# Performance work log

Hardware: AMD Instinct MI355X
Metric: run time of the kernel (lower is better)

The kernel has to match this reference:

```python
import jax, jax.numpy as jnp
import numpy as np

N_NODES = 50000
N_EDGES = 800000
D_IN = 128
D_H = 128
D_OUT = 1
N_GRAPHS = 64
BN_EPS = 1e-5


def _lin(key, i, o):
    return jax.random.normal(key, (i, o), jnp.float32) / np.float32(np.sqrt(i))


def setup_inputs() -> dict:
    key = jax.random.key(0)
    ks = jax.random.split(key, 40)
    inp = {}
    inp["x"] = jax.random.normal(ks[0], (N_NODES, D_IN), jnp.float32)
    inp["edge_index"] = jax.random.randint(ks[1], (2, N_EDGES), 0, N_NODES)
    inp["batch"] = jnp.sort(jax.random.randint(ks[2], (N_NODES,), 0, N_GRAPHS))
    dims = [D_IN, D_H, D_H]
    ki = 3
    for l in range(3):
        inp[f"l{l}_W1"] = _lin(ks[ki], dims[l], D_H); ki += 1
        inp[f"l{l}_b1"] = jnp.zeros((D_H,), jnp.float32)
        inp[f"l{l}_W2"] = _lin(ks[ki], D_H, D_H); ki += 1
        inp[f"l{l}_b2"] = jnp.zeros((D_H,), jnp.float32)
        inp[f"l{l}_g"] = jnp.ones((D_H,), jnp.float32)
        inp[f"l{l}_beta"] = jnp.zeros((D_H,), jnp.float32)
    inp["p_W1"] = _lin(ks[ki], D_H * 3, D_H); ki += 1
    inp["p_b1"] = jnp.zeros((D_H,), jnp.float32)
    inp["p_g"] = jnp.ones((D_H,), jnp.float32)
    inp["p_beta"] = jnp.zeros((D_H,), jnp.float32)
    inp["p_W2"] = _lin(ks[ki], D_H, D_OUT); ki += 1
    inp["p_b2"] = jnp.zeros((D_OUT,), jnp.float32)
    return inp


def _bn(h, g, b):
    # training-mode BatchNorm1d: biased batch statistics over dim 0
    m = h.mean(0)
    v = h.var(0)
    return (h - m) * (g / jnp.sqrt(v + BN_EPS)) + b


def _gin_conv(x, src, dst, W1, b1, W2, b2):
    # scatter-add neighbor aggregation: messages x[src] summed into dst
    agg = jax.ops.segment_sum(x[src], dst, num_segments=N_NODES)
    h = x + agg  # eps = 0 (GINConv default)
    h = jax.nn.relu(h @ W1 + b1)
    return h @ W2 + b2


def reference(x, edge_index, batch,
              l0_W1, l0_b1, l0_W2, l0_b2, l0_g, l0_beta,
              l1_W1, l1_b1, l1_W2, l1_b2, l1_g, l1_beta,
              l2_W1, l2_b1, l2_W2, l2_b2, l2_g, l2_beta,
              p_W1, p_b1, p_g, p_beta, p_W2, p_b2):
    src, dst = edge_index[0], edge_index[1]
    layers = [
        (l0_W1, l0_b1, l0_W2, l0_b2, l0_g, l0_beta),
        (l1_W1, l1_b1, l1_W2, l1_b2, l1_g, l1_beta),
        (l2_W1, l2_b1, l2_W2, l2_b2, l2_g, l2_beta),
    ]
    h = x
    h_list = []
    for (W1, b1, W2, b2, g, beta) in layers:
        h = _gin_conv(h, src, dst, W1, b1, W2, b2)
        h = jax.nn.relu(_bn(h, g, beta))
        # dropout: identity in eval mode
        h_list.append(h)
    # global mean pool per layer, then concat
    cnt = jax.ops.segment_sum(jnp.ones((N_NODES,), jnp.float32), batch,
                              num_segments=N_GRAPHS)
    cnt = jnp.maximum(cnt, 1.0)[:, None]
    pooled = [jax.ops.segment_sum(hh, batch, num_segments=N_GRAPHS) / cnt
              for hh in h_list]
    z = jnp.concatenate(pooled, axis=1)  # [G, 3*D_H]
    # prediction MLP: fc1 -> relu -> bn -> fc2 (dropout identity)
    z = jax.nn.relu(z @ p_W1 + p_b1)
    z = _bn(z, p_g, p_beta)
    return z @ p_W2 + p_b2  # [G, D_OUT]
```

## Files before the change

kernel.cpp:

```cpp
#include <hip/hip_runtime.h>

#define NN 50000
#define NE 800000
#define D  128
#define NG 64
#define BN_EPS 1e-5f
#define SCAN_B 196

typedef __attribute__((ext_vector_type(8))) short short8;
typedef __attribute__((ext_vector_type(4))) float f32x4;

static __device__ inline unsigned short f2bf_rn(float f) {
  unsigned u = __float_as_uint(f);
  unsigned r = (u + 0x7FFF + ((u >> 16) & 1)) >> 16;
  return (unsigned short)r;
}
static __device__ inline float bf2f(unsigned short h) {
  return __uint_as_float((unsigned)h << 16);
}

__global__ void k_hist(const int* __restrict__ dst, int* __restrict__ counts) {
  int e = blockIdx.x * blockDim.x + threadIdx.x;
  if (e < NE) atomicAdd(&counts[dst[e]], 1);
}

__global__ void k_scan1(const int* __restrict__ counts, int* __restrict__ bsum) {
  const int t = threadIdx.x;
  const int i = blockIdx.x * 256 + t;
  int v = (i < NN) ? counts[i] : 0;
  #pragma unroll
  for (int d = 32; d >= 1; d >>= 1) v += __shfl_xor(v, d, 64);
  __shared__ int ws[4];
  if ((t & 63) == 0) ws[t >> 6] = v;
  __syncthreads();
  if (t == 0) bsum[blockIdx.x] = ws[0] + ws[1] + ws[2] + ws[3];
}

__global__ void k_scan2(const int* __restrict__ bsum, int* __restrict__ boff,
                        int* __restrict__ offs) {
  const int t = threadIdx.x, lane = t & 63, w = t >> 6;
  int v = (t < SCAN_B) ? bsum[t] : 0;
  int s = v;
  #pragma unroll
  for (int d = 1; d < 64; d <<= 1) { int u = __shfl_up(s, d, 64); if (lane >= d) s += u; }
  __shared__ int ws[4];
  if (lane == 63) ws[w] = s;
  __syncthreads();
  int add = 0;
  for (int k = 0; k < w; ++k) add += ws[k];
  if (t < SCAN_B) boff[t] = add + s - v;
  if (t == SCAN_B - 1) offs[NN] = add + s;
}

__global__ void k_scan3(const int* __restrict__ counts, const int* __restrict__ boff,
                        int* __restrict__ offs) {
  const int t = threadIdx.x, lane = t & 63, w = t >> 6;
  const int i = blockIdx.x * 256 + t;
  int v = (i < NN) ? counts[i] : 0;
  int s = v;
  #pragma unroll
  for (int d = 1; d < 64; d <<= 1) { int u = __shfl_up(s, d, 64); if (lane >= d) s += u; }
  __shared__ int ws[4];
  if (lane == 63) ws[w] = s;
  __syncthreads();
  int add = 0;
  for (int k = 0; k < w; ++k) add += ws[k];
  if (i < NN) offs[i] = boff[blockIdx.x] + add + s - v;
}

__global__ void k_scatter(const int* __restrict__ src, const int* __restrict__ dst,
                          const int* __restrict__ offs, int* __restrict__ cursor,
                          int* __restrict__ esrc) {
  int e = blockIdx.x * blockDim.x + threadIdx.x;
  if (e < NE) {
    int d = dst[e];
    int p = offs[d] + atomicAdd(&cursor[d], 1);
    esrc[p] = src[e];
  }
}

__global__ void k_gbounds(const int* __restrict__ batch, int* __restrict__ gstart) {
  const int g = threadIdx.x;
  if (g > NG) return;
  int lo = 0, hi = NN;
  while (lo < hi) { int mid = (lo + hi) >> 1; if (batch[mid] < g) lo = mid + 1; else hi = mid; }
  gstart[g] = lo;
}

__global__ __launch_bounds__(256) void k_cvt(const float* __restrict__ X,
                                             unsigned long long* __restrict__ Xb) {
  const int n4 = NN * D / 4;
  for (int i = blockIdx.x * blockDim.x + threadIdx.x; i < n4; i += gridDim.x * blockDim.x) {
    float4 v = ((const float4*)X)[i];
    unsigned long long p = (unsigned long long)f2bf_rn(v.x) |
                           ((unsigned long long)f2bf_rn(v.y) << 16) |
                           ((unsigned long long)f2bf_rn(v.z) << 32) |
                           ((unsigned long long)f2bf_rn(v.w) << 48);
    Xb[i] = p;
  }
}

struct WPtrs { const float* w[6]; };
__global__ void k_prep6(WPtrs ws, short* __restrict__ wb) {
  const int widx = blockIdx.y;
  const float* __restrict__ W = ws.w[widx];
  short* __restrict__ Wh = wb + (size_t)(widx * 2) * 16384;
  short* __restrict__ Wl = Wh + 16384;
  const int idx = blockIdx.x * 256 + threadIdx.x;
  const int k = idx >> 7, c = idx & 127;
  const float v = W[idx];
  const unsigned short h = f2bf_rn(v);
  const unsigned short lo = f2bf_rn(v - bf2f(h));
  const int o = ((k >> 5) * 128 + c) * 32 + (k & 31);
  Wh[o] = (short)h;
  Wl[o] = (short)lo;
}

template<bool BN>
__global__ __launch_bounds__(256) void k_aggregate(const unsigned* __restrict__ Hb,
                                                   const int* __restrict__ offs,
                                                   const int* __restrict__ esrc,
                                                   const float* __restrict__ scale,
                                                   const float* __restrict__ shift,
                                                   unsigned* __restrict__ AGGh,
                                                   unsigned* __restrict__ AGGl) {
  const int node = blockIdx.x * 4 + (threadIdx.x >> 6);
  const int lane = threadIdx.x & 63;
  float2 sc = make_float2(1.f, 1.f), sh = make_float2(0.f, 0.f);
  if (BN) { sc = ((const float2*)scale)[lane]; sh = ((const float2*)shift)[lane]; }

  auto rd = [&](int r) -> float2 {
    const unsigned u = Hb[r * 64 + lane];
    float2 v = make_float2(bf2f((unsigned short)u), bf2f((unsigned short)(u >> 16)));
    if (BN) {
      v.x = fmaxf(fmaf(v.x, sc.x, sh.x), 0.f);
      v.y = fmaxf(fmaf(v.y, sc.y, sh.y), 0.f);
    }
    return v;
  };

  float2 acc = rd(node);
  const int b = offs[node], e = offs[node + 1];
  int i = b;
  for (; i + 4 <= e; i += 4) {
    const int s0 = esrc[i], s1 = esrc[i + 1], s2 = esrc[i + 2], s3 = esrc[i + 3];
    const float2 v0 = rd(s0), v1 = rd(s1), v2 = rd(s2), v3 = rd(s3);
    acc.x += (v0.x + v1.x) + (v2.x + v3.x);
    acc.y += (v0.y + v1.y) + (v2.y + v3.y);
  }
  for (; i < e; ++i) {
    const float2 v = rd(esrc[i]);
    acc.x += v.x; acc.y += v.y;
  }
  const unsigned short hx = f2bf_rn(acc.x), hy = f2bf_rn(acc.y);
  AGGh[node * 64 + lane] = (unsigned)hx | ((unsigned)hy << 16);
  const unsigned short lx = f2bf_rn(acc.x - bf2f(hx)), ly = f2bf_rn(acc.y - bf2f(hy));
  AGGl[node * 64 + lane] = (unsigned)lx | ((unsigned)ly << 16);
}

__global__ __launch_bounds__(256, 3) void k_mlp(const short* __restrict__ AGGh,
                                                const short* __restrict__ AGGl,
                                                const short* __restrict__ W1h, const short* __restrict__ W1l,
                                                const short* __restrict__ W2h, const short* __restrict__ W2l,
                                                const float* __restrict__ b1, const float* __restrict__ b2,
                                                short* __restrict__ Hb,
                                                float* __restrict__ sums, float* __restrict__ sumsq) {
  __shared__ __align__(16) short sC1h[64 * 136];
  __shared__ __align__(16) short sC1l[64 * 136];

  const int t = threadIdx.x;
  const int l = t & 63, w = t >> 6;
  const int lr = l & 15, fq = l >> 4;
  const int lk = fq * 8;
  const int row0 = blockIdx.x * 64;
  const int arow = row0 + w * 16 + lr;
  const bool rowok = arow < NN;

  f32x4 acc[8];
  #pragma unroll
  for (int ct = 0; ct < 8; ++ct) acc[ct] = (f32x4)(0.f);
  #pragma unroll 1
  for (int kc = 0; kc < 4; ++kc) {
    short8 ah = (short8)(0), al = (short8)(0);
    if (rowok) {
      ah = *(const short8*)(AGGh + (size_t)arow * D + kc * 32 + lk);
      al = *(const short8*)(AGGl + (size_t)arow * D + kc * 32 + lk);
    }
    short8 bh[8], bl[8];
    #pragma unroll
    for (int ct = 0; ct < 8; ++ct) {
      bh[ct] = *(const short8*)(W1h + (kc * 128 + ct * 16 + lr) * 32 + lk);
      bl[ct] = *(const short8*)(W1l + (kc * 128 + ct * 16 + lr) * 32 + lk);
    }
    #pragma unroll
    for (int ct = 0; ct < 8; ++ct) {
      acc[ct] = __builtin_amdgcn_mfma_f32_16x16x32_bf16(ah, bh[ct], acc[ct], 0, 0, 0);
      acc[ct] = __builtin_amdgcn_mfma_f32_16x16x32_bf16(al, bh[ct], acc[ct], 0, 0, 0);
      acc[ct] = __builtin_amdgcn_mfma_f32_16x16x32_bf16(ah, bl[ct], acc[ct], 0, 0, 0);
    }
  }

  #pragma unroll
  for (int ct = 0; ct < 8; ++ct) {
    const float bb = b1[ct * 16 + lr];
    #pragma unroll
    for (int j = 0; j < 4; ++j) {
      const int r = w * 16 + fq * 4 + j;
      const float v = fmaxf(acc[ct][j] + bb, 0.f);
      const unsigned short h = f2bf_rn(v);
      sC1h[r * 136 + ct * 16 + lr] = (short)h;
      sC1l[r * 136 + ct * 16 + lr] = (short)f2bf_rn(v - bf2f(h));
    }
  }
  __syncthreads();

  f32x4 acc2[8];
  #pragma unroll
  for (int ct = 0; ct < 8; ++ct) acc2[ct] = (f32x4)(0.f);
  #pragma unroll 1
  for (int kc = 0; kc < 4; ++kc) {
    const short8 ah = *(const short8*)(sC1h + (w * 16 + lr) * 136 + kc * 32 + lk);
    const short8 al = *(const short8*)(sC1l + (w * 16 + lr) * 136 + kc * 32 + lk);
    short8 bh[8], bl[8];
    #pragma unroll
    for (int ct = 0; ct < 8; ++ct) {
      bh[ct] = *(const short8*)(W2h + (kc * 128 + ct * 16 + lr) * 32 + lk);
      bl[ct] = *(const short8*)(W2l + (kc * 128 + ct * 16 + lr) * 32 + lk);
    }
    #pragma unroll
    for (int ct = 0; ct < 8; ++ct) {
      acc2[ct] = __builtin_amdgcn_mfma_f32_16x16x32_bf16(ah, bh[ct], acc2[ct], 0, 0, 0);
      acc2[ct] = __builtin_amdgcn_mfma_f32_16x16x32_bf16(al, bh[ct], acc2[ct], 0, 0, 0);
      acc2[ct] = __builtin_amdgcn_mfma_f32_16x16x32_bf16(ah, bl[ct], acc2[ct], 0, 0, 0);
    }
  }

  float ps[8], pq[8];
  #pragma unroll
  for (int ct = 0; ct < 8; ++ct) { ps[ct] = 0.f; pq[ct] = 0.f; }
  #pragma unroll
  for (int ct = 0; ct < 8; ++ct) {
    const float bb = b2[ct * 16 + lr];
    #pragma unroll
    for (int j = 0; j < 4; ++j) {
      const int gr = row0 + w * 16 + fq * 4 + j;
      if (gr < NN) {
        const float v = acc2[ct][j] + bb;
        Hb[(size_t)gr * D + ct * 16 + lr] = (short)f2bf_rn(v);
        ps[ct] += v; pq[ct] += v * v;
      }
    }
  }
  __syncthreads();
  float* red  = (float*)sC1h;
  float* redq = (float*)sC1l;
  const int grp = w * 4 + fq;
  #pragma unroll
  for (int ct = 0; ct < 8; ++ct) {
    red [grp * 128 + ct * 16 + lr] = ps[ct];
    redq[grp * 128 + ct * 16 + lr] = pq[ct];
  }
  __syncthreads();
  if (t < 128) {
    float s = 0.f, q = 0.f;
    #pragma unroll
    for (int g2 = 0; g2 < 16; ++g2) { s += red[g2 * 128 + t]; q += redq[g2 * 128 + t]; }
    atomicAdd(&sums[t], s);
    atomicAdd(&sumsq[t], q);
  }
}

__global__ void k_stats(const float* __restrict__ sums, const float* __restrict__ sumsq,
                        const float* __restrict__ g, const float* __restrict__ beta,
                        float* __restrict__ scale, float* __restrict__ shift) {
  const int c = threadIdx.x;
  const float m   = sums[c] / (float)NN;
  const float var = sumsq[c] / (float)NN - m * m;
  const float sc  = g[c] / sqrtf(var + BN_EPS);
  scale[c] = sc;
  shift[c] = beta[c] - m * sc;
}

__global__ __launch_bounds__(256) void k_pool(const unsigned short* __restrict__ Hb,
                                              const float* __restrict__ scale,
                                              const float* __restrict__ shift,
                                              const int* __restrict__ gstart,
                                              float* __restrict__ pooled, int lofs) {
  const int g = blockIdx.y;
  const int s = gstart[g], e = gstart[g + 1];
  const int t = threadIdx.x, c = t & 127, half = t >> 7;
  const float sc = scale[c], sh = shift[c];
  const int len = e - s;
  const int nchunk = (int)gridDim.x;
  const int per = (len + nchunk - 1) / nchunk;
  const int r0 = s + (int)blockIdx.x * per;
  const int r1 = min(e, r0 + per);
  float sum = 0.f;
  for (int r = r0 + half; r < r1; r += 2)
    sum += fmaxf(fmaf(bf2f(Hb[r * D + c]), sc, sh), 0.f);
  __shared__ float red[256];
  red[t] = sum;
  __syncthreads();
  if (t < 128) atomicAdd(&pooled[g * 384 + lofs + c], red[t] + red[t + 128]);
}

__global__ __launch_bounds__(128) void k_fc1(const float* __restrict__ pooled,
                                             const int* __restrict__ gstart,
                                             const float* __restrict__ W1,
                                             const float* __restrict__ b1,
                                             float* __restrict__ z1) {
  const int g = blockIdx.x, j = threadIdx.x;
  __shared__ float p[384];
  const float cnt = (float)(gstart[g + 1] - gstart[g]);
  const float inv = 1.f / fmaxf(cnt, 1.f);
  for (int k = j; k < 384; k += 128) p[k] = pooled[g * 384 + k] * inv;
  __syncthreads();
  float acc = b1[j];
  #pragma unroll 8
  for (int k = 0; k < 384; ++k) acc = fmaf(p[k], W1[k * 128 + j], acc);
  z1[g * 128 + j] = fmaxf(acc, 0.f);
}

__global__ __launch_bounds__(128) void k_head(const float* __restrict__ z1,
                                              const float* __restrict__ g,
                                              const float* __restrict__ beta,
                                              const float* __restrict__ W2,
                                              const float* __restrict__ b2,
                                              float* __restrict__ out) {
  __shared__ float z2[NG][129];
  __shared__ float w2s[128];
  const int j = threadIdx.x;
  w2s[j] = W2[j];
  float vals[NG];
  float s = 0.f, q = 0.f;
  for (int gg = 0; gg < NG; ++gg) {
    float v = z1[gg * 128 + j];
    vals[gg] = v; s += v; q += v * v;
  }
  const float m   = s / (float)NG;
  const float var = q / (float)NG - m * m;
  const float sc  = g[j] / sqrtf(var + BN_EPS);
  const float sh  = beta[j] - m * sc;
  for (int gg = 0; gg < NG; ++gg) z2[gg][j] = vals[gg] * sc + sh;
  __syncthreads();
  if (j < NG) {
    float acc = b2[0];
    #pragma unroll 8
    for (int k = 0; k < 128; ++k) acc += z2[j][k] * w2s[k];
    out[j] = acc;
  }
}

extern "C" void kernel_launch(void* const* d_in, const int* in_sizes, int n_in,
                              void* d_out, int out_size, void* d_ws, size_t ws_size,
                              hipStream_t stream) {
  const float* x     = (const float*)d_in[0];
  const int*   e_src = (const int*)d_in[1];
  const int*   e_dst = e_src + NE;
  const int*   batch = (const int*)d_in[2];
  const float *lW1[3], *lb1[3], *lW2[3], *lb2[3], *lg[3], *lbeta[3];
  for (int l = 0; l < 3; ++l) {
    lW1[l]   = (const float*)d_in[3 + 6 * l + 0];
    lb1[l]   = (const float*)d_in[3 + 6 * l + 1];
    lW2[l]   = (const float*)d_in[3 + 6 * l + 2];
    lb2[l]   = (const float*)d_in[3 + 6 * l + 3];
    lg[l]    = (const float*)d_in[3 + 6 * l + 4];
    lbeta[l] = (const float*)d_in[3 + 6 * l + 5];
  }
  const float* pW1   = (const float*)d_in[21];
  const float* pb1   = (const float*)d_in[22];
  const float* pg    = (const float*)d_in[23];
  const float* pbeta = (const float*)d_in[24];
  const float* pW2   = (const float*)d_in[25];
  const float* pb2   = (const float*)d_in[26];
  float* out = (float*)d_out;

  char* w = (char*)d_ws;
  auto alloc = [&](size_t bytes) { char* p = w; w += (bytes + 255) & ~(size_t)255; return p; };
  short* AGGh   = (short*)alloc((size_t)NN * D * 2);
  short* AGGl   = (short*)alloc((size_t)NN * D * 2);
  short* Hb0    = (short*)alloc((size_t)NN * D * 2);
  short* Hb1    = (short*)alloc((size_t)NN * D * 2);
  short* xb     = Hb1;
  int*   counts = (int*)alloc((size_t)NN * 4);
  int*   cursor = (int*)alloc((size_t)NN * 4);
  int*   offs   = (int*)alloc((size_t)(NN + 1) * 4);
  int*   esrc   = (int*)alloc((size_t)NE * 4);
  int*   bsum   = (int*)alloc((size_t)SCAN_B * 4);
  int*   boff   = (int*)alloc((size_t)SCAN_B * 4);
  int*   gstart = (int*)alloc((size_t)(NG + 1) * 4);
  float* stats  = (float*)alloc((size_t)4 * 128 * 4);
  float* sums = stats, *sumsq = stats + 128, *scale = stats + 256, *shift = stats + 384;
  float* pooled = (float*)alloc((size_t)NG * 384 * 4);
  float* z1     = (float*)alloc((size_t)NG * 128 * 4);
  short* wb     = (short*)alloc((size_t)12 * 32768);

  hipMemsetAsync(counts, 0, (size_t)NN * 4, stream);
  hipMemsetAsync(cursor, 0, (size_t)NN * 4, stream);
  hipMemsetAsync(pooled, 0, (size_t)NG * 384 * 4, stream);

  k_hist   <<<(NE + 255) / 256, 256, 0, stream>>>(e_dst, counts);
  k_scan1  <<<SCAN_B, 256, 0, stream>>>(counts, bsum);
  k_scan2  <<<1, 256, 0, stream>>>(bsum, boff, offs);
  k_scan3  <<<SCAN_B, 256, 0, stream>>>(counts, boff, offs);
  k_scatter<<<(NE + 255) / 256, 256, 0, stream>>>(e_src, e_dst, offs, cursor, esrc);
  k_gbounds<<<1, 128, 0, stream>>>(batch, gstart);
  k_cvt    <<<1024, 256, 0, stream>>>(x, (unsigned long long*)xb);

  WPtrs ws;
  ws.w[0] = lW1[0]; ws.w[1] = lW2[0];
  ws.w[2] = lW1[1]; ws.w[3] = lW2[1];
  ws.w[4] = lW1[2]; ws.w[5] = lW2[2];
  k_prep6<<<dim3(64, 6), 256, 0, stream>>>(ws, wb);
  auto plane = [&](int widx, int hilo) { return wb + (size_t)(widx * 2 + hilo) * 16384; };

  short* Hbuf[2] = {Hb0, Hb1};
  const int mlp_grid = (NN + 63) / 64;
  for (int l = 0; l < 3; ++l) {
    if (l == 0)
      k_aggregate<false><<<NN / 4, 256, 0, stream>>>((const unsigned*)xb, offs, esrc,
                                                     nullptr, nullptr,
                                                     (unsigned*)AGGh, (unsigned*)AGGl);
    else
      k_aggregate<true><<<NN / 4, 256, 0, stream>>>((const unsigned*)Hbuf[(l - 1) & 1], offs, esrc,
                                                    scale, shift,
                                                    (unsigned*)AGGh, (unsigned*)AGGl);
    hipMemsetAsync(sums, 0, 2 * 128 * 4, stream);
    k_mlp<<<mlp_grid, 256, 0, stream>>>(AGGh, AGGl,
                                        plane(2 * l, 0), plane(2 * l, 1),
                                        plane(2 * l + 1, 0), plane(2 * l + 1, 1),
                                        lb1[l], lb2[l], Hbuf[l & 1], sums, sumsq);
    k_stats<<<1, 128, 0, stream>>>(sums, sumsq, lg[l], lbeta[l], scale, shift);
    k_pool <<<dim3(8, NG), 256, 0, stream>>>((const unsigned short*)Hbuf[l & 1], scale, shift,
                                             gstart, pooled, l * 128);
  }

  k_fc1 <<<NG, 128, 0, stream>>>(pooled, gstart, pW1, pb1, z1);
  k_head<<<1, 128, 0, stream>>>(z1, pg, pbeta, pW2, pb2, out);
}
```

Before: 465.9 us.

## Fold BN stats into consumers and software-pipeline MLP weight loads

Removes the single-block k_stats kernel per layer by computing BatchNorm scale/shift directly from sums/sumsq inside the aggregate and pool kernels. The MLP kernel's two GEMMs are fully unrolled, with all A fragments preloaded and weight fragments double-buffered in half-tiles so loads overlap with MFMA work. This cuts launch overhead and load latency stalls, at the cost of redundant per-thread rsqrt work and higher register pressure that may affect occupancy.

```diff
diff --git a/kernel.cpp b/kernel.cpp
--- a/kernel.cpp
+++ b/kernel.cpp
@@ -120,14 +120,26 @@
 __global__ __launch_bounds__(256) void k_aggregate(const unsigned* __restrict__ Hb,
                                                    const int* __restrict__ offs,
                                                    const int* __restrict__ esrc,
-                                                   const float* __restrict__ scale,
-                                                   const float* __restrict__ shift,
+                                                   const float* __restrict__ sums,
+                                                   const float* __restrict__ sumsq,
+                                                   const float* __restrict__ gw,
+                                                   const float* __restrict__ beta,
                                                    unsigned* __restrict__ AGGh,
                                                    unsigned* __restrict__ AGGl) {
   const int node = blockIdx.x * 4 + (threadIdx.x >> 6);
   const int lane = threadIdx.x & 63;
   float2 sc = make_float2(1.f, 1.f), sh = make_float2(0.f, 0.f);
-  if (BN) { sc = ((const float2*)scale)[lane]; sh = ((const float2*)shift)[lane]; }
+  if (BN) {
+    const float2 s2 = ((const float2*)sums)[lane];
+    const float2 q2 = ((const float2*)sumsq)[lane];
+    const float2 g2 = ((const float2*)gw)[lane];
+    const float2 b2 = ((const float2*)beta)[lane];
+    const float mx = s2.x * (1.f / NN), my = s2.y * (1.f / NN);
+    sc.x = g2.x / sqrtf(q2.x * (1.f / NN) - mx * mx + BN_EPS);
+    sc.y = g2.y / sqrtf(q2.y * (1.f / NN) - my * my + BN_EPS);
+    sh.x = b2.x - mx * sc.x;
+    sh.y = b2.y - my * sc.y;
+  }
 
   auto rd = [&](int r) -> float2 {
     const unsigned u = Hb[r * 64 + lane];
@@ -158,6 +170,18 @@
   AGGl[node * 64 + lane] = (unsigned)lx | ((unsigned)ly << 16);
 }
 
+#define LDW4(BH, BL, WPH, WPL, kc, half)                                        \
+  { _Pragma("unroll") for (int q = 0; q < 4; ++q) {                             \
+      const int ct = (half) * 4 + q;                                            \
+      BH[q] = *(const short8*)((WPH) + ((kc) * 128 + ct * 16 + lr) * 32 + lk);  \
+      BL[q] = *(const short8*)((WPL) + ((kc) * 128 + ct * 16 + lr) * 32 + lk); } }
+
+#define MM4(ACC, AH, AL, BH, BL, half)                                                          \
+  { _Pragma("unroll") for (int q = 0; q < 4; ++q) {                                             \
+      ACC[(half)*4+q] = __builtin_amdgcn_mfma_f32_16x16x32_bf16(AH, BH[q], ACC[(half)*4+q],0,0,0); \
+      ACC[(half)*4+q] = __builtin_amdgcn_mfma_f32_16x16x32_bf16(AL, BH[q], ACC[(half)*4+q],0,0,0); \
+      ACC[(half)*4+q] = __builtin_amdgcn_mfma_f32_16x16x32_bf16(AH, BL[q], ACC[(half)*4+q],0,0,0); } }
+
 __global__ __launch_bounds__(256, 3) void k_mlp(const short* __restrict__ AGGh,
                                                 const short* __restrict__ AGGl,
                                                 const short* __restrict__ W1h, const short* __restrict__ W1l,
@@ -179,25 +203,38 @@
   f32x4 acc[8];
   #pragma unroll
   for (int ct = 0; ct < 8; ++ct) acc[ct] = (f32x4)(0.f);
-  #pragma unroll 1
-  for (int kc = 0; kc < 4; ++kc) {
-    short8 ah = (short8)(0), al = (short8)(0);
-    if (rowok) {
-      ah = *(const short8*)(AGGh + (size_t)arow * D + kc * 32 + lk);
-      al = *(const short8*)(AGGl + (size_t)arow * D + kc * 32 + lk);
-    }
-    short8 bh[8], bl[8];
-    #pragma unroll
-    for (int ct = 0; ct < 8; ++ct) {
-      bh[ct] = *(const short8*)(W1h + (kc * 128 + ct * 16 + lr) * 32 + lk);
-      bl[ct] = *(const short8*)(W1l + (kc * 128 + ct * 16 + lr) * 32 + lk);
-    }
-    #pragma unroll
-    for (int ct = 0; ct < 8; ++ct) {
-      acc[ct] = __builtin_amdgcn_mfma_f32_16x16x32_bf16(ah, bh[ct], acc[ct], 0, 0, 0);
-      acc[ct] = __builtin_amdgcn_mfma_f32_16x16x32_bf16(al, bh[ct], acc[ct], 0, 0, 0);
-      acc[ct] = __builtin_amdgcn_mfma_f32_16x16x32_bf16(ah, bl[ct], acc[ct], 0, 0, 0);
-    }
+
+  short8 a0h, a0l, a1h, a1l, a2h, a2l, a3h, a3l;
+  {
+    const short8 z = (short8)(0);
+    const size_t base = (size_t)arow * D + lk;
+    a0h = rowok ? *(const short8*)(AGGh + base +  0) : z;
+    a0l = rowok ? *(const short8*)(AGGl + base +  0) : z;
+    a1h = rowok ? *(const short8*)(AGGh + base + 32) : z;
+    a1l = rowok ? *(const short8*)(AGGl + base + 32) : z;
+    a2h = rowok ? *(const short8*)(AGGh + base + 64) : z;
+    a2l = rowok ? *(const short8*)(AGGl + base + 64) : z;
+    a3h = rowok ? *(const short8*)(AGGh + base + 96) : z;
+    a3l = rowok ? *(const short8*)(AGGl + base + 96) : z;
+  }
+  {
+    short8 bhA[4], blA[4], bhB[4], blB[4];
+    LDW4(bhA, blA, W1h, W1l, 0, 0);
+    LDW4(bhB, blB, W1h, W1l, 0, 1);
+    MM4(acc, a0h, a0l, bhA, blA, 0);
+    LDW4(bhA, blA, W1h, W1l, 1, 0);
+    MM4(acc, a0h, a0l, bhB, blB, 1);
+    LDW4(bhB, blB, W1h, W1l, 1, 1);
+    MM4(acc, a1h, a1l, bhA, blA, 0);
+    LDW4(bhA, blA, W1h, W1l, 2, 0);
+    MM4(acc, a1h, a1l, bhB, blB, 1);
+    LDW4(bhB, blB, W1h, W1l, 2, 1);
+    MM4(acc, a2h, a2l, bhA, blA, 0);
+    LDW4(bhA, blA, W1h, W1l, 3, 0);
+    MM4(acc, a2h, a2l, bhB, blB, 1);
+    LDW4(bhB, blB, W1h, W1l, 3, 1);
+    MM4(acc, a3h, a3l, bhA, blA, 0);
+    MM4(acc, a3h, a3l, bhB, blB, 1);
   }
 
   #pragma unroll
@@ -217,22 +254,33 @@
   f32x4 acc2[8];
   #pragma unroll
   for (int ct = 0; ct < 8; ++ct) acc2[ct] = (f32x4)(0.f);
-  #pragma unroll 1
-  for (int kc = 0; kc < 4; ++kc) {
-    const short8 ah = *(const short8*)(sC1h + (w * 16 + lr) * 136 + kc * 32 + lk);
-    const short8 al = *(const short8*)(sC1l + (w * 16 + lr) * 136 + kc * 32 + lk);
-    short8 bh[8], bl[8];
-    #pragma unroll
-    for (int ct = 0; ct < 8; ++ct) {
-      bh[ct] = *(const short8*)(W2h + (kc * 128 + ct * 16 + lr) * 32 + lk);
-      bl[ct] = *(const short8*)(W2l + (kc * 128 + ct * 16 + lr) * 32 + lk);
-    }
-    #pragma unroll
-    for (int ct = 0; ct < 8; ++ct) {
-      acc2[ct] = __builtin_amdgcn_mfma_f32_16x16x32_bf16(ah, bh[ct], acc2[ct], 0, 0, 0);
-      acc2[ct] = __builtin_amdgcn_mfma_f32_16x16x32_bf16(al, bh[ct], acc2[ct], 0, 0, 0);
-      acc2[ct] = __builtin_amdgcn_mfma_f32_16x16x32_bf16(ah, bl[ct], acc2[ct], 0, 0, 0);
-    }
+  {
+    const int cbase = (w * 16 + lr) * 136 + lk;
+    const short8 c0h = *(const short8*)(sC1h + cbase +  0);
+    const short8 c0l = *(const short8*)(sC1l + cbase +  0);
+    const short8 c1h = *(const short8*)(sC1h + cbase + 32);
+    const short8 c1l = *(const short8*)(sC1l + cbase + 32);
+    const short8 c2h = *(const short8*)(sC1h + cbase + 64);
+    const short8 c2l = *(const short8*)(sC1l + cbase + 64);
+    const short8 c3h = *(const short8*)(sC1h + cbase + 96);
+    const short8 c3l = *(const short8*)(sC1l + cbase + 96);
+    short8 bhA[4], blA[4], bhB[4], blB[4];
+    LDW4(bhA, blA, W2h, W2l, 0, 0);
+    LDW4(bhB, blB, W2h, W2l, 0, 1);
+    MM4(acc2, c0h, c0l, bhA, blA, 0);
+    LDW4(bhA, blA, W2h, W2l, 1, 0);
+    MM4(acc2, c0h, c0l, bhB, blB, 1);
+    LDW4(bhB, blB, W2h, W2l, 1, 1);
+    MM4(acc2, c1h, c1l, bhA, blA, 0);
+    LDW4(bhA, blA, W2h, W2l, 2, 0);
+    MM4(acc2, c1h, c1l, bhB, blB, 1);
+    LDW4(bhB, blB, W2h, W2l, 2, 1);
+    MM4(acc2, c2h, c2l, bhA, blA, 0);
+    LDW4(bhA, blA, W2h, W2l, 3, 0);
+    MM4(acc2, c2h, c2l, bhB, blB, 1);
+    LDW4(bhB, blB, W2h, W2l, 3, 1);
+    MM4(acc2, c3h, c3l, bhA, blA, 0);
+    MM4(acc2, c3h, c3l, bhB, blB, 1);
   }
 
   float ps[8], pq[8];
@@ -270,26 +318,19 @@
   }
 }
 
-__global__ void k_stats(const float* __restrict__ sums, const float* __restrict__ sumsq,
-                        const float* __restrict__ g, const float* __restrict__ beta,
-                        float* __restrict__ scale, float* __restrict__ shift) {
-  const int c = threadIdx.x;
-  const float m   = sums[c] / (float)NN;
-  const float var = sumsq[c] / (float)NN - m * m;
-  const float sc  = g[c] / sqrtf(var + BN_EPS);
-  scale[c] = sc;
-  shift[c] = beta[c] - m * sc;
-}
-
 __global__ __launch_bounds__(256) void k_pool(const unsigned short* __restrict__ Hb,
-                                              const float* __restrict__ scale,
-                                              const float* __restrict__ shift,
+                                              const float* __restrict__ sums,
+                                              const float* __restrict__ sumsq,
+                                              const float* __restrict__ gw,
+                                              const float* __restrict__ beta,
                                               const int* __restrict__ gstart,
                                               float* __restrict__ pooled, int lofs) {
   const int g = blockIdx.y;
   const int s = gstart[g], e = gstart[g + 1];
   const int t = threadIdx.x, c = t & 127, half = t >> 7;
-  const float sc = scale[c], sh = shift[c];
+  const float m  = sums[c] * (1.f / NN);
+  const float sc = gw[c] / sqrtf(sumsq[c] * (1.f / NN) - m * m + BN_EPS);
+  const float sh = beta[c] - m * sc;
   const int len = e - s;
   const int nchunk = (int)gridDim.x;
   const int per = (len + nchunk - 1) / nchunk;
@@ -389,8 +430,8 @@
   int*   bsum   = (int*)alloc((size_t)SCAN_B * 4);
   int*   boff   = (int*)alloc((size_t)SCAN_B * 4);
   int*   gstart = (int*)alloc((size_t)(NG + 1) * 4);
-  float* stats  = (float*)alloc((size_t)4 * 128 * 4);
-  float* sums = stats, *sumsq = stats + 128, *scale = stats + 256, *shift = stats + 384;
+  float* stats  = (float*)alloc((size_t)2 * 128 * 4);
+  float* sums = stats, *sumsq = stats + 128;
   float* pooled = (float*)alloc((size_t)NG * 384 * 4);
   float* z1     = (float*)alloc((size_t)NG * 128 * 4);
   short* wb     = (short*)alloc((size_t)12 * 32768);
@@ -419,19 +460,19 @@
   for (int l = 0; l < 3; ++l) {
     if (l == 0)
       k_aggregate<false><<<NN / 4, 256, 0, stream>>>((const unsigned*)xb, offs, esrc,
-                                                     nullptr, nullptr,
+                                                     nullptr, nullptr, nullptr, nullptr,
                                                      (unsigned*)AGGh, (unsigned*)AGGl);
     else
       k_aggregate<true><<<NN / 4, 256, 0, stream>>>((const unsigned*)Hbuf[(l - 1) & 1], offs, esrc,
-                                                    scale, shift,
+                                                    sums, sumsq, lg[l - 1], lbeta[l - 1],
                                                     (unsigned*)AGGh, (unsigned*)AGGl);
     hipMemsetAsync(sums, 0, 2 * 128 * 4, stream);
     k_mlp<<<mlp_grid, 256, 0, stream>>>(AGGh, AGGl,
                                         plane(2 * l, 0), plane(2 * l, 1),
                                         plane(2 * l + 1, 0), plane(2 * l + 1, 1),
                                         lb1[l], lb2[l], Hbuf[l & 1], sums, sumsq);
-    k_stats<<<1, 128, 0, stream>>>(sums, sumsq, lg[l], lbeta[l], scale, shift);
-    k_pool <<<dim3(8, NG), 256, 0, stream>>>((const unsigned short*)Hbuf[l & 1], scale, shift,
+    k_pool <<<dim3(8, NG), 256, 0, stream>>>((const unsigned short*)Hbuf[l & 1],
+                                             sums, sumsq, lg[l], lbeta[l],
                                              gstart, pooled, l * 128);
   }
 
```

Measured after the change: 471.2 us. No clear change (+1.2%).
